# Kernel tuning notes

Measured on AMD Instinct MI355X. Metric: run time of the kernel, lower is better.

The kernel has to match this reference:

```python
import jax, jax.numpy as jnp
import numpy as np

N = 50000
E = 1_600_000
IN_C = 128
HID = 64
HEADS = 2
OUT_C = 16
NEG_SLOPE = 0.2
EPS = 1e-16


def setup_inputs() -> dict:
    key = jax.random.key(0)
    ks = jax.random.split(key, 10)
    x = jax.random.normal(ks[0], (N, IN_C), dtype=jnp.float32)
    edge_index = jax.random.randint(ks[1], (2, E), 0, N, dtype=jnp.int64)
    # layer 1: in -> HEADS * HID, concat=True
    s1 = 1.0 / np.sqrt(IN_C)
    W1 = jax.random.normal(ks[2], (IN_C, HEADS * HID), dtype=jnp.float32) * s1
    att_src1 = jax.random.normal(ks[3], (HEADS, HID), dtype=jnp.float32) * (1.0 / np.sqrt(HID))
    att_dst1 = jax.random.normal(ks[4], (HEADS, HID), dtype=jnp.float32) * (1.0 / np.sqrt(HID))
    b1 = jnp.zeros((HEADS * HID,), dtype=jnp.float32)
    # layer 2: HEADS*HID -> OUT_C, heads=1
    s2 = 1.0 / np.sqrt(HEADS * HID)
    W2 = jax.random.normal(ks[5], (HEADS * HID, OUT_C), dtype=jnp.float32) * s2
    att_src2 = jax.random.normal(ks[6], (1, OUT_C), dtype=jnp.float32) * (1.0 / np.sqrt(OUT_C))
    att_dst2 = jax.random.normal(ks[7], (1, OUT_C), dtype=jnp.float32) * (1.0 / np.sqrt(OUT_C))
    b2 = jnp.zeros((OUT_C,), dtype=jnp.float32)
    return {"x": x, "W1": W1, "att_src1": att_src1, "att_dst1": att_dst1, "b1": b1,
            "W2": W2, "att_src2": att_src2, "att_dst2": att_dst2, "b2": b2,
            "edge_index": edge_index}


def gat_conv(x, edge_index, W, att_src, att_dst, bias, heads, out_ch):
    """PyG-style GATConv: per-head linear, additive attention, softmax over
    incoming edges of each destination node, scatter-add aggregation."""
    n = x.shape[0]
    src, dst = edge_index[0], edge_index[1]
    h = (x @ W).reshape(n, heads, out_ch)                # [N,H,C]
    a_src = jnp.einsum('nhc,hc->nh', h, att_src)          # [N,H]
    a_dst = jnp.einsum('nhc,hc->nh', h, att_dst)          # [N,H]
    e = a_src[src] + a_dst[dst]                           # [E,H]
    e = jnp.where(e >= 0, e, NEG_SLOPE * e)               # LeakyReLU(0.2)
    e_max = jax.ops.segment_max(e, dst, num_segments=n)   # [N,H]
    e_max = jax.lax.stop_gradient(jnp.where(jnp.isfinite(e_max), e_max, 0.0))
    e_exp = jnp.exp(e - e_max[dst])                       # [E,H]
    denom = jax.ops.segment_sum(e_exp, dst, num_segments=n)  # [N,H]
    alpha = e_exp / (denom[dst] + EPS)                    # [E,H]
    msg = h[src] * alpha[:, :, None]                      # [E,H,C] (dominant traffic)
    out = jax.ops.segment_sum(msg, dst, num_segments=n)   # [N,H,C]
    return out.reshape(n, heads * out_ch) + bias


def reference(x, W1, att_src1, att_dst1, b1, W2, att_src2, att_dst2, b2, edge_index):
    h = gat_conv(x, edge_index, W1, att_src1, att_dst1, b1, HEADS, HID)
    h = jax.nn.elu(h)
    h = gat_conv(h, edge_index, W2, att_src2, att_dst2, b2, 1, OUT_C)
    return jax.nn.softmax(h, axis=1)
```

## Files before the change

### kernel.cpp

```cpp
#include <hip/hip_runtime.h>
#include <hip/hip_fp16.h>
#include <cstdint>
#include <cstddef>

#define N_NODES 50000
#define N_EDGES 1600000
#define NEG_SLOPE 0.2f
#define GAT_EPS 1e-16f

#define NCHUNK 128
#define CE (N_EDGES / NCHUNK)
#define NBKT 196
#define GEMM_BLOCKS 782

typedef _Float16 half8v __attribute__((ext_vector_type(8)));
typedef _Float16 half4v __attribute__((ext_vector_type(4)));
typedef float f32x4 __attribute__((ext_vector_type(4)));



__global__ __launch_bounds__(256) void k_gh(
    const float* __restrict__ x, const float* __restrict__ W1,
    const float* __restrict__ W2, const float* __restrict__ b1,
    const float* __restrict__ att_src, const float* __restrict__ att_dst,
    _Float16* __restrict__ h1p, float* __restrict__ a_src, float* __restrict__ a_dst,
    const int* __restrict__ ei, int* __restrict__ coarse,
    float* __restrict__ w2tp, float* __restrict__ b1p) {
    __shared__ __align__(16) char smem[34816];
    int t = threadIdx.x;
    int b = blockIdx.x;
    if (b == GEMM_BLOCKS + NCHUNK) {
        for (int i = t; i < 2112; i += 256) {
            int j = i / 132, kp = i % 132;
            float v = 0.f;
            if (kp < 128) {
                int real = (kp & 7) * 16 + (kp >> 3);
                v = W2[real * 16 + j];
            }
            w2tp[i] = v;
        }
        if (t < 128) {
            int real = (t & 7) * 16 + (t >> 3);
            b1p[t] = b1[real];
        }
        return;
    }
    if (b >= GEMM_BLOCKS) {
        int* h = (int*)smem;
        int g = b - GEMM_BLOCKS;
        int wv = t >> 6;
        for (int i = t; i < 1024; i += 256) h[i] = 0;
        __syncthreads();
        int* hw = h + (wv << 8);
        int e0 = g * CE;
        for (int e = e0 + t; e < e0 + CE; e += 256)
            atomicAdd(&hw[ei[N_EDGES + e] >> 8], 1);
        __syncthreads();
        if (t < NBKT) coarse[g * NBKT + t] = h[t] + h[256 + t] + h[512 + t] + h[768 + t];
        return;
    }
    _Float16* wl = (_Float16*)smem;
    for (int j = t; j < 16384; j += 256) {
        int k = j >> 7, c = j & 127;
        wl[c * 136 + k] = (_Float16)W1[j];
    }
    __syncthreads();
    int wv = t >> 6, lane = t & 63;
    int m = lane & 15, q = lane >> 4;
    int nb = b * 64 + wv * 16;
    int grow = nb + m;
    const float* xrow = x + (size_t)((grow < N_NODES) ? grow : (N_NODES - 1)) * 128;
    f32x4 acc[8];
#pragma unroll
    for (int ct = 0; ct < 8; ++ct) acc[ct] = (f32x4){0.f, 0.f, 0.f, 0.f};
#pragma unroll
    for (int kc = 0; kc < 4; ++kc) {
        float4 u0 = *(const float4*)(xrow + kc * 32 + q * 8);
        float4 u1 = *(const float4*)(xrow + kc * 32 + q * 8 + 4);
        half8v a;
        a[0] = (_Float16)u0.x; a[1] = (_Float16)u0.y;
        a[2] = (_Float16)u0.z; a[3] = (_Float16)u0.w;
        a[4] = (_Float16)u1.x; a[5] = (_Float16)u1.y;
        a[6] = (_Float16)u1.z; a[7] = (_Float16)u1.w;
#pragma unroll
        for (int ct = 0; ct < 8; ++ct) {
            half8v bf = *(const half8v*)(wl + (ct * 16 + m) * 136 + kc * 32 + q * 8);
            acc[ct] = __builtin_amdgcn_mfma_f32_16x16x32_f16(a, bf, acc[ct], 0, 0, 0);
        }
    }
    float att_s[8], att_d[8];
#pragma unroll
    for (int ct = 0; ct < 8; ++ct) {
        att_s[ct] = att_src[ct * 16 + m];
        att_d[ct] = att_dst[ct * 16 + m];
    }
#pragma unroll
    for (int r = 0; r < 4; ++r) {
        int gn = nb + q * 4 + r;
        half8v hv;
        float ps0 = 0.f, ps1 = 0.f, pd0 = 0.f, pd1 = 0.f;
#pragma unroll
        for (int ct = 0; ct < 8; ++ct) {
            float v = acc[ct][r];
            hv[ct] = (_Float16)v;
            if (ct < 4) { ps0 += v * att_s[ct]; pd0 += v * att_d[ct]; }
            else        { ps1 += v * att_s[ct]; pd1 += v * att_d[ct]; }
        }
#pragma unroll
        for (int off = 8; off >= 1; off >>= 1) {
            ps0 += __shfl_xor(ps0, off, 64);
            ps1 += __shfl_xor(ps1, off, 64);
            pd0 += __shfl_xor(pd0, off, 64);
            pd1 += __shfl_xor(pd1, off, 64);
        }
        if (gn < N_NODES) {
            *(half8v*)(h1p + (size_t)gn * 128 + m * 8) = hv;
            if (m == 0) {
                a_src[gn * 2 + 0] = ps0;
                a_src[gn * 2 + 1] = ps1;
                a_dst[gn * 2 + 0] = pd0;
                a_dst[gn * 2 + 1] = pd1;
            }
        }
    }
}


__global__ __launch_bounds__(1024) void k_cscan(const int* __restrict__ coarse,
                                                int* __restrict__ cbase,
                                                int* __restrict__ bb,
                                                int* __restrict__ row_start) {
    __shared__ int cl[NBKT * NCHUNK];
    __shared__ int btot[256];
    __shared__ int bbase[NBKT];
    __shared__ int wt4[4];
    int t = threadIdx.x;
    for (int i = t; i < NBKT * NCHUNK; i += 1024) cl[i] = coarse[i];
    __syncthreads();
    if (t < 256) {
        int s = 0;
        if (t < NBKT)
            for (int g = 0; g < NCHUNK; ++g) s += cl[g * NBKT + t];
        btot[t] = s;
        int lane = t & 63, w = t >> 6;
        int x = s;
#pragma unroll
        for (int off = 1; off < 64; off <<= 1) {
            int y = __shfl_up(x, off, 64);
            if (lane >= off) x += y;
        }
        if (lane == 63) wt4[w] = x;
        __syncthreads();
        int woff = 0;
        for (int i = 0; i < w; ++i) woff += wt4[i];
        if (t < NBKT) bbase[t] = woff + x - s;
    } else {
        __syncthreads();
    }
    __syncthreads();
    if (t < NBKT) {
        int run = bbase[t];
        bb[t] = run;
        for (int g = 0; g < NCHUNK; ++g) {
            cbase[g * NBKT + t] = run;
            run += cl[g * NBKT + t];
        }
    }
    if (t == 0) { bb[NBKT] = N_EDGES; row_start[N_NODES] = N_EDGES; }
}

__global__ __launch_bounds__(256) void k_partition(const int* __restrict__ ei,
                                                   const int* __restrict__ cbase,
                                                   unsigned int* __restrict__ part) {
    __shared__ int loc[NBKT];
    int t = threadIdx.x, g = blockIdx.x;
    if (t < NBKT) loc[t] = cbase[g * NBKT + t];
    __syncthreads();
    int e0 = g * CE;
    for (int e = e0 + t; e < e0 + CE; e += 256) {
        int s = ei[e], d = ei[N_EDGES + e];
        int slot = atomicAdd(&loc[d >> 8], 1);
        part[slot] = ((unsigned int)d << 16) | (unsigned int)s;
    }
}

__global__ __launch_bounds__(256) void k_local(const unsigned int* __restrict__ part,
                                               const int* __restrict__ bb,
                                               const float* __restrict__ a_src1,
                                               const float* __restrict__ a_dst1,
                                               int* __restrict__ row_start,
                                               int* __restrict__ csrc,
                                               float2* __restrict__ cw) {
    __shared__ int hist[256];
    __shared__ int fillv[256];
    __shared__ float2 adl[256];
    __shared__ int wtot[4];
    int t = threadIdx.x, b = blockIdx.x;
    int n0 = b << 8;
    int es = bb[b], ee = bb[b + 1];
    hist[t] = 0;
    if (n0 + t < N_NODES) adl[t] = ((const float2*)a_dst1)[n0 + t];
    __syncthreads();
    for (int e = es + t; e < ee; e += 256) atomicAdd(&hist[(part[e] >> 16) - n0], 1);
    __syncthreads();
    int lane = t & 63, w = t >> 6;
    int v = hist[t], x = v;
#pragma unroll
    for (int off = 1; off < 64; off <<= 1) {
        int y = __shfl_up(x, off, 64);
        if (lane >= off) x += y;
    }
    if (lane == 63) wtot[w] = x;
    __syncthreads();
    int woff = 0;
    for (int i = 0; i < w; ++i) woff += wtot[i];
    int excl = woff + x - v;
    if (n0 + t < N_NODES) row_start[n0 + t] = es + excl;
    fillv[t] = excl;
    __syncthreads();
    for (int e = es + t; e < ee; e += 256) {
        unsigned int sd = part[e];
        int s = (int)(sd & 0xFFFFu);
        int j = (int)(sd >> 16) - n0;
        int slot = es + atomicAdd(&fillv[j], 1);
        float2 as = ((const float2*)a_src1)[s];
        float2 ad = adl[j];
        float e0 = as.x + ad.x; e0 = (e0 >= 0.f) ? e0 : NEG_SLOPE * e0;
        float e1 = as.y + ad.y; e1 = (e1 >= 0.f) ? e1 : NEG_SLOPE * e1;
        csrc[slot] = s;
        cw[slot] = make_float2(expf(e0), expf(e1));
    }
}


__global__ __launch_bounds__(256) void k_agg1f(
    const int* __restrict__ row_start, const int* __restrict__ csrc,
    const float2* __restrict__ cw,
    const _Float16* __restrict__ h1p, const float* __restrict__ b1p,
    const float* __restrict__ w2tp,
    const float* __restrict__ att_src2, const float* __restrict__ att_dst2,
    float* __restrict__ h2, float* __restrict__ as2, float* __restrict__ ad2) {
    __shared__ float w2l[16 * 132];
    __shared__ float rows[4][128];
    __shared__ int4 elds[4][64];
    int t = threadIdx.x;
    for (int i = t; i < 528; i += 256) ((float4*)w2l)[i] = ((const float4*)w2tp)[i];
    __syncthreads();
    int wv = t >> 6, lane = t & 63;
    int d = blockIdx.x * 4 + wv;
    int row = row_start[d], end = row_start[d + 1];
    int m16 = lane & 15;
    int qt = lane >> 4;
    uint32_t moff = (uint32_t)m16 * 16u;
    const char* hbase = (const char*)h1p;
    float den0 = 0.f, den1 = 0.f;
    float acc[8];
#pragma unroll
    for (int i = 0; i < 8; ++i) acc[i] = 0.f;
    for (int base = row; base < end; base += 64) {
        int m = end - base;
        if (m > 64) m = 64;
        int idx = base + lane;
        int idxc = (idx < end) ? idx : (end - 1);
        int s = csrc[idxc];
        float2 wv2 = cw[idxc];
        if (idx >= end) { wv2.x = 0.f; wv2.y = 0.f; }
        elds[wv][lane] = make_int4(s, __float_as_int(wv2.x), __float_as_int(wv2.y), 0);
        int nc = (m + 3) >> 2;
        auto step = [&](int p) {
            int4 md = elds[wv][p * 4 + qt];
            float w0 = __int_as_float(md.y);
            float w1 = __int_as_float(md.z);
            uint32_t off = ((uint32_t)md.x << 8) + moff;
            half8v hv = *(const half8v*)(hbase + off);
            den0 += w0;
            den1 += w1;
            acc[0] += w0 * (float)hv[0];
            acc[1] += w0 * (float)hv[1];
            acc[2] += w0 * (float)hv[2];
            acc[3] += w0 * (float)hv[3];
            acc[4] += w1 * (float)hv[4];
            acc[5] += w1 * (float)hv[5];
            acc[6] += w1 * (float)hv[6];
            acc[7] += w1 * (float)hv[7];
        };
        int p = 0;
        for (; p + 4 <= nc; p += 4) {
            step(p); step(p + 1); step(p + 2); step(p + 3);
        }
        for (; p < nc; ++p) step(p);
    }
#pragma unroll
    for (int i = 0; i < 8; ++i) {
        acc[i] += __shfl_xor(acc[i], 16, 64);
        acc[i] += __shfl_xor(acc[i], 32, 64);
    }
    den0 += __shfl_xor(den0, 16, 64);
    den0 += __shfl_xor(den0, 32, 64);
    den1 += __shfl_xor(den1, 16, 64);
    den1 += __shfl_xor(den1, 32, 64);
    float inv0 = 1.f / (den0 + GAT_EPS);
    float inv1 = 1.f / (den1 + GAT_EPS);
    {
        int cbase2 = qt * 2;
        float inv = (cbase2 < 4) ? inv0 : inv1;
        float2 bv = *(const float2*)(b1p + m16 * 8 + cbase2);
        float oa = acc[cbase2] * inv + bv.x;
        float ob = acc[cbase2 + 1] * inv + bv.y;
        oa = (oa > 0.f) ? oa : expm1f(oa);
        ob = (ob > 0.f) ? ob : expm1f(ob);
        *(float2*)(&rows[wv][m16 * 8 + cbase2]) = make_float2(oa, ob);
    }
    int j = lane & 15, q = lane >> 4;
    const float* r = rows[wv];
    const float* wt = &w2l[j * 132];
    int k0 = q * 32;
    float acc2 = 0.f;
#pragma unroll
    for (int sI = 0; sI < 8; ++sI) {
        int sp = ((sI + q) & 7) * 4;
        float4 rv = *(const float4*)(r + k0 + sp);
        float4 w4 = *(const float4*)(wt + k0 + sp);
        acc2 += rv.x * w4.x + rv.y * w4.y + rv.z * w4.z + rv.w * w4.w;
    }
    acc2 += __shfl_xor(acc2, 16, 64);
    acc2 += __shfl_xor(acc2, 32, 64);
    if (lane < 16) {
        h2[(size_t)d * 16 + j] = acc2;
        float ps = acc2 * att_src2[j];
        float pd = acc2 * att_dst2[j];
#pragma unroll
        for (int off = 8; off >= 1; off >>= 1) {
            ps += __shfl_xor(ps, off, 64);
            pd += __shfl_xor(pd, off, 64);
        }
        if (lane == 0) { as2[d] = ps; ad2[d] = pd; }
    }
}


__global__ __launch_bounds__(256) void k_agg2(
    const int* __restrict__ row_start, const int* __restrict__ csrc,
    const float* __restrict__ h2, const float* __restrict__ as2,
    const float* __restrict__ ad2, const float* __restrict__ b2,
    float* __restrict__ out) {
    __shared__ int2 elds[4][64];
    int t = threadIdx.x;
    int wv = t >> 6, lane = t & 63;
    int d = blockIdx.x * 4 + wv;
    int row = row_start[d], end = row_start[d + 1];
    float ad = ad2[d];
    int g16 = lane >> 2;
    int cq = lane & 3;
    float den = 0.f;
    float ax = 0.f, ay = 0.f, az = 0.f, aw = 0.f;
    for (int base = row; base < end; base += 64) {
        int m = end - base;
        if (m > 64) m = 64;
        int idx = base + lane;
        int idxc = (idx < end) ? idx : (end - 1);
        int s = csrc[idxc];
        float w = 0.f;
        if (idx < end) {
            float e = as2[s] + ad;
            e = (e >= 0.f) ? e : NEG_SLOPE * e;
            w = expf(e);
        }
        den += w;
        elds[wv][lane] = make_int2(s, __float_as_int(w));
        int nc = (m + 15) >> 4;
        auto step = [&](int p) {
            int2 md = elds[wv][p * 16 + g16];
            float wj = __int_as_float(md.y);
            float4 hv = *(const float4*)(h2 + (size_t)md.x * 16 + cq * 4);
            ax += wj * hv.x;
            ay += wj * hv.y;
            az += wj * hv.z;
            aw += wj * hv.w;
        };
        int p = 0;
        for (; p + 4 <= nc; p += 4) {
            step(p); step(p + 1); step(p + 2); step(p + 3);
        }
        for (; p < nc; ++p) step(p);
    }
#pragma unroll
    for (int off = 32; off >= 1; off >>= 1) den += __shfl_xor(den, off, 64);
#pragma unroll
    for (int off = 4; off <= 32; off <<= 1) {
        ax += __shfl_xor(ax, off, 64);
        ay += __shfl_xor(ay, off, 64);
        az += __shfl_xor(az, off, 64);
        aw += __shfl_xor(aw, off, 64);
    }
    float inv = 1.f / (den + GAT_EPS);
    const float4 b4 = *(const float4*)(b2 + cq * 4);
    float v0 = ax * inv + b4.x;
    float v1 = ay * inv + b4.y;
    float v2 = az * inv + b4.z;
    float v3 = aw * inv + b4.w;
    float mmax = fmaxf(fmaxf(v0, v1), fmaxf(v2, v3));
    mmax = fmaxf(mmax, __shfl_xor(mmax, 1, 64));
    mmax = fmaxf(mmax, __shfl_xor(mmax, 2, 64));
    float e0 = expf(v0 - mmax);
    float e1 = expf(v1 - mmax);
    float e2 = expf(v2 - mmax);
    float e3 = expf(v3 - mmax);
    float sum = e0 + e1 + e2 + e3;
    sum += __shfl_xor(sum, 1, 64);
    sum += __shfl_xor(sum, 2, 64);
    float isum = 1.f / sum;
    if (g16 == 0)
        *(float4*)(out + (size_t)d * 16 + cq * 4) =
            make_float4(e0 * isum, e1 * isum, e2 * isum, e3 * isum);
}


extern "C" void kernel_launch(void* const* d_in, const int* in_sizes, int n_in,
                              void* d_out, int out_size, void* d_ws, size_t ws_size,
                              hipStream_t stream) {
    const float* x        = (const float*)d_in[0];
    const float* W1       = (const float*)d_in[1];
    const float* att_src1 = (const float*)d_in[2];
    const float* att_dst1 = (const float*)d_in[3];
    const float* b1       = (const float*)d_in[4];
    const float* W2       = (const float*)d_in[5];
    const float* att_src2 = (const float*)d_in[6];
    const float* att_dst2 = (const float*)d_in[7];
    const float* b2       = (const float*)d_in[8];
    const int*   ei       = (const int*)d_in[9];

    char* p = (char*)d_ws;
    auto alloc = [&](size_t bytes) {
        char* r = p;
        p += (bytes + 255) & ~(size_t)255;
        return r;
    };
    _Float16* h1p  = (_Float16*)alloc(sizeof(_Float16) * (size_t)N_NODES * 128);
    float* w2tp    = (float*)alloc(sizeof(float) * 16 * 132);
    float* b1p     = (float*)alloc(sizeof(float) * 128);
    float* h2      = (float*)alloc(sizeof(float) * (size_t)N_NODES * 16);
    float* a_src   = (float*)alloc(sizeof(float) * N_NODES * 2);
    float* a_dst   = (float*)alloc(sizeof(float) * N_NODES * 2);
    float* as2     = (float*)alloc(sizeof(float) * N_NODES);
    float* ad2     = (float*)alloc(sizeof(float) * N_NODES);
    int* coarse    = (int*)alloc(sizeof(int) * NBKT * NCHUNK);
    int* cbase     = (int*)alloc(sizeof(int) * NBKT * NCHUNK);
    int* bb        = (int*)alloc(sizeof(int) * (NBKT + 1));
    int* row_start = (int*)alloc(sizeof(int) * (N_NODES + 1));
    unsigned int* part = (unsigned int*)alloc(sizeof(unsigned int) * (size_t)N_EDGES);
    int* csrc      = (int*)alloc(sizeof(int) * (size_t)N_EDGES);
    float2* cw     = (float2*)alloc(sizeof(float2) * (size_t)N_EDGES);

    k_gh<<<GEMM_BLOCKS + NCHUNK + 1, 256, 0, stream>>>(x, W1, W2, b1, att_src1, att_dst1,
                                                       h1p, a_src, a_dst, ei, coarse, w2tp, b1p);
    k_cscan<<<1, 1024, 0, stream>>>(coarse, cbase, bb, row_start);
    k_partition<<<NCHUNK, 256, 0, stream>>>(ei, cbase, part);
    k_local<<<NBKT, 256, 0, stream>>>(part, bb, a_src, a_dst, row_start, csrc, cw);
    k_agg1f<<<N_NODES / 4, 256, 0, stream>>>(row_start, csrc, cw, h1p, b1p, w2tp, att_src2, att_dst2, h2, as2, ad2);
    k_agg2<<<N_NODES / 4, 256, 0, stream>>>(row_start, csrc, h2, as2, ad2, b2, (float*)d_out);
}
```

Baseline: 251.1 us.

## Widen edge partition grid with global atomics and vectorize histogram loads

The partition kernel now runs as a 2048-block grid-stride loop that claims slots with global atomics on the per-chunk bucket cursors, instead of 128 blocks each using shared-memory cursors. This is meant to fix the low occupancy of the partition step. The histogram pass reads destination indices as int4, the scan reads coarse counts straight from global memory with 256 threads, and the local CSR build uses 512-thread blocks. The cost is heavy global atomic contention on about 25k counters. Edge order inside each bucket also becomes nondeterministic, though results should stay the same apart from float summation order.

```diff
diff --git a/kernel.cpp b/kernel.cpp
--- a/kernel.cpp
+++ b/kernel.cpp
@@ -52,9 +52,14 @@
         for (int i = t; i < 1024; i += 256) h[i] = 0;
         __syncthreads();
         int* hw = h + (wv << 8);
-        int e0 = g * CE;
-        for (int e = e0 + t; e < e0 + CE; e += 256)
-            atomicAdd(&hw[ei[N_EDGES + e] >> 8], 1);
+        const int4* d4 = (const int4*)(ei + N_EDGES + g * CE);
+        for (int i = t; i < CE / 4; i += 256) {
+            int4 v = d4[i];
+            atomicAdd(&hw[v.x >> 8], 1);
+            atomicAdd(&hw[v.y >> 8], 1);
+            atomicAdd(&hw[v.z >> 8], 1);
+            atomicAdd(&hw[v.w >> 8], 1);
+        }
         __syncthreads();
         if (t < NBKT) coarse[g * NBKT + t] = h[t] + h[256 + t] + h[512 + t] + h[768 + t];
         return;
@@ -126,65 +131,53 @@
 }
 
 
-__global__ __launch_bounds__(1024) void k_cscan(const int* __restrict__ coarse,
-                                                int* __restrict__ cbase,
-                                                int* __restrict__ bb,
-                                                int* __restrict__ row_start) {
-    __shared__ int cl[NBKT * NCHUNK];
-    __shared__ int btot[256];
-    __shared__ int bbase[NBKT];
+__global__ __launch_bounds__(256) void k_cscan(const int* __restrict__ coarse,
+                                               int* __restrict__ cbase,
+                                               int* __restrict__ bb,
+                                               int* __restrict__ row_start) {
     __shared__ int wt4[4];
     int t = threadIdx.x;
-    for (int i = t; i < NBKT * NCHUNK; i += 1024) cl[i] = coarse[i];
-    __syncthreads();
-    if (t < 256) {
-        int s = 0;
-        if (t < NBKT)
-            for (int g = 0; g < NCHUNK; ++g) s += cl[g * NBKT + t];
-        btot[t] = s;
-        int lane = t & 63, w = t >> 6;
-        int x = s;
-#pragma unroll
-        for (int off = 1; off < 64; off <<= 1) {
-            int y = __shfl_up(x, off, 64);
-            if (lane >= off) x += y;
-        }
-        if (lane == 63) wt4[w] = x;
-        __syncthreads();
-        int woff = 0;
-        for (int i = 0; i < w; ++i) woff += wt4[i];
-        if (t < NBKT) bbase[t] = woff + x - s;
-    } else {
-        __syncthreads();
-    }
-    __syncthreads();
+    int s = 0;
+    if (t < NBKT)
+        for (int g = 0; g < NCHUNK; ++g) s += coarse[g * NBKT + t];
+    int lane = t & 63, w = t >> 6;
+    int x = s;
+#pragma unroll
+    for (int off = 1; off < 64; off <<= 1) {
+        int y = __shfl_up(x, off, 64);
+        if (lane >= off) x += y;
+    }
+    if (lane == 63) wt4[w] = x;
+    __syncthreads();
+    int woff = 0;
+    for (int i = 0; i < w; ++i) woff += wt4[i];
     if (t < NBKT) {
-        int run = bbase[t];
+        int run = woff + x - s;
         bb[t] = run;
         for (int g = 0; g < NCHUNK; ++g) {
             cbase[g * NBKT + t] = run;
-            run += cl[g * NBKT + t];
+            run += coarse[g * NBKT + t];
         }
     }
     if (t == 0) { bb[NBKT] = N_EDGES; row_start[N_NODES] = N_EDGES; }
 }
 
+
 __global__ __launch_bounds__(256) void k_partition(const int* __restrict__ ei,
-                                                   const int* __restrict__ cbase,
+                                                   int* __restrict__ cbase,
                                                    unsigned int* __restrict__ part) {
-    __shared__ int loc[NBKT];
-    int t = threadIdx.x, g = blockIdx.x;
-    if (t < NBKT) loc[t] = cbase[g * NBKT + t];
-    __syncthreads();
-    int e0 = g * CE;
-    for (int e = e0 + t; e < e0 + CE; e += 256) {
+    int tid = blockIdx.x * 256 + threadIdx.x;
+    int stride = gridDim.x * 256;
+    for (int e = tid; e < N_EDGES; e += stride) {
         int s = ei[e], d = ei[N_EDGES + e];
-        int slot = atomicAdd(&loc[d >> 8], 1);
+        int g = e / CE;
+        int slot = atomicAdd(&cbase[g * NBKT + (d >> 8)], 1);
         part[slot] = ((unsigned int)d << 16) | (unsigned int)s;
     }
 }
 
-__global__ __launch_bounds__(256) void k_local(const unsigned int* __restrict__ part,
+
+__global__ __launch_bounds__(512) void k_local(const unsigned int* __restrict__ part,
                                                const int* __restrict__ bb,
                                                const float* __restrict__ a_src1,
                                                const float* __restrict__ a_dst1,
@@ -198,27 +191,34 @@
     int t = threadIdx.x, b = blockIdx.x;
     int n0 = b << 8;
     int es = bb[b], ee = bb[b + 1];
-    hist[t] = 0;
-    if (n0 + t < N_NODES) adl[t] = ((const float2*)a_dst1)[n0 + t];
-    __syncthreads();
-    for (int e = es + t; e < ee; e += 256) atomicAdd(&hist[(part[e] >> 16) - n0], 1);
-    __syncthreads();
-    int lane = t & 63, w = t >> 6;
-    int v = hist[t], x = v;
-#pragma unroll
-    for (int off = 1; off < 64; off <<= 1) {
-        int y = __shfl_up(x, off, 64);
-        if (lane >= off) x += y;
-    }
-    if (lane == 63) wtot[w] = x;
-    __syncthreads();
-    int woff = 0;
-    for (int i = 0; i < w; ++i) woff += wtot[i];
-    int excl = woff + x - v;
-    if (n0 + t < N_NODES) row_start[n0 + t] = es + excl;
-    fillv[t] = excl;
-    __syncthreads();
-    for (int e = es + t; e < ee; e += 256) {
+    if (t < 256) {
+        hist[t] = 0;
+        if (n0 + t < N_NODES) adl[t] = ((const float2*)a_dst1)[n0 + t];
+    }
+    __syncthreads();
+    for (int e = es + t; e < ee; e += 512) atomicAdd(&hist[(part[e] >> 16) - n0], 1);
+    __syncthreads();
+    int v = 0, x = 0, w = 0;
+    if (t < 256) {
+        int lane = t & 63; w = t >> 6;
+        v = hist[t]; x = v;
+#pragma unroll
+        for (int off = 1; off < 64; off <<= 1) {
+            int y = __shfl_up(x, off, 64);
+            if (lane >= off) x += y;
+        }
+        if (lane == 63) wtot[w] = x;
+    }
+    __syncthreads();
+    if (t < 256) {
+        int woff = 0;
+        for (int i = 0; i < w; ++i) woff += wtot[i];
+        int excl = woff + x - v;
+        if (n0 + t < N_NODES) row_start[n0 + t] = es + excl;
+        fillv[t] = excl;
+    }
+    __syncthreads();
+    for (int e = es + t; e < ee; e += 512) {
         unsigned int sd = part[e];
         int s = (int)(sd & 0xFFFFu);
         int j = (int)(sd >> 16) - n0;
@@ -454,9 +454,9 @@
 
     k_gh<<<GEMM_BLOCKS + NCHUNK + 1, 256, 0, stream>>>(x, W1, W2, b1, att_src1, att_dst1,
                                                        h1p, a_src, a_dst, ei, coarse, w2tp, b1p);
-    k_cscan<<<1, 1024, 0, stream>>>(coarse, cbase, bb, row_start);
-    k_partition<<<NCHUNK, 256, 0, stream>>>(ei, cbase, part);
-    k_local<<<NBKT, 256, 0, stream>>>(part, bb, a_src, a_dst, row_start, csrc, cw);
+    k_cscan<<<1, 256, 0, stream>>>(coarse, cbase, bb, row_start);
+    k_partition<<<2048, 256, 0, stream>>>(ei, cbase, part);
+    k_local<<<NBKT, 512, 0, stream>>>(part, bb, a_src, a_dst, row_start, csrc, cw);
     k_agg1f<<<N_NODES / 4, 256, 0, stream>>>(row_start, csrc, cw, h1p, b1p, w2tp, att_src2, att_dst2, h2, as2, ad2);
     k_agg2<<<N_NODES / 4, 256, 0, stream>>>(row_start, csrc, h2, as2, ad2, b2, (float*)d_out);
 }
```

Measured after the change: 276.0 us. 10.0% more time.
